# Optimization experiments

Measured on AMD Instinct MI355X. Metric: run time of the kernel, lower is better.

The kernel has to match this reference:

```python
import jax, jax.numpy as jnp
import numpy as np

N = 20000        # nodes per type (ant, user)
E = 400000       # edges per relation
F_IN = 128       # args.user_num -> input feature dim
H = 10           # attention heads
D1, D2 = 16, 32  # per-head out channels of HGT layers 1 and 2
H1, H2 = H * D1, H * D2  # 160, 320


def _segment_softmax(logit, dst, n):
    m = jax.ops.segment_max(logit, dst, num_segments=n)
    e = jnp.exp(logit - m[dst])
    s = jax.ops.segment_sum(e, dst, num_segments=n)
    return e / (s[dst] + 1e-16)


def _hgt_layer(x_a, x_u, ei_au, ea_au, ei_ua, ea_ua,
               kw, kb, qw, qb, vw, vb, arel, mrel, prel, ew, eb, alw, alb, D):
    # per-node-type K/Q/V projections, reshaped to [N, H, D]
    def proj(x, w, b, i):
        return (x @ w[i] + b[i]).reshape(x.shape[0], H, D)
    k_a, q_a, v_a = proj(x_a, kw, kb, 0), proj(x_a, qw, qb, 0), proj(x_a, vw, vb, 0)
    k_u, q_u, v_u = proj(x_u, kw, kb, 1), proj(x_u, qw, qb, 1), proj(x_u, vw, vb, 1)
    scale = 1.0 / jnp.sqrt(jnp.float32(D))

    def relation(k_s, v_s, q_d, ei, ea, r, n_dst):
        # apply per-relation matrices at node granularity (cheaper than per-edge)
        kr = jnp.einsum('nhd,hde->nhe', k_s, arel[r])
        vr = jnp.einsum('nhd,hde->nhe', v_s, mrel[r])
        src, dst = ei[0], ei[1]
        # [E, H] attention logits: HGT dot-product * relation prior + edge-attr term
        logit = (q_d[dst] * kr[src]).sum(-1) * scale * prel[r] + ea @ ew[r] + eb[r]
        a = _segment_softmax(logit, dst, n_dst)
        msg = vr[src] * a[..., None]                        # [E, H, D]
        out = jax.ops.segment_sum(msg, dst, num_segments=n_dst)
        return out.reshape(n_dst, H * D)

    agg_u = relation(k_a, v_a, q_u, ei_au, ea_au, 0, x_u.shape[0])  # ant -> user
    agg_a = relation(k_u, v_u, q_a, ei_ua, ea_ua, 1, x_a.shape[0])  # user -> ant
    out_a = jax.nn.gelu(agg_a) @ alw[0] + alb[0]
    out_u = jax.nn.gelu(agg_u) @ alw[1] + alb[1]
    return out_a, out_u


def _bn(x, g, b):
    mu = x.mean(0)
    var = x.var(0)
    return (x - mu) / jnp.sqrt(var + 1e-5) * g + b


def _forward(x_ant, x_user, ea_au, ea_ua,
             l1_kw, l1_kb, l1_qw, l1_qb, l1_vw, l1_vb, l1_arel, l1_mrel, l1_prel, l1_ew, l1_eb, l1_alw, l1_alb,
             l2_kw, l2_kb, l2_qw, l2_qb, l2_vw, l2_vb, l2_arel, l2_mrel, l2_prel, l2_ew, l2_eb, l2_alw, l2_alb,
             lin1_w, lin1_b, bn_g, bn_b, lin2_wa, lin2_ba, lin2_wu, lin2_bu,
             ei_au, ei_ua):
    a, u = _hgt_layer(x_ant, x_user, ei_au, ea_au, ei_ua, ea_ua,
                      l1_kw, l1_kb, l1_qw, l1_qb, l1_vw, l1_vb,
                      l1_arel, l1_mrel, l1_prel, l1_ew, l1_eb, l1_alw, l1_alb, D1)
    a, u = jax.nn.elu(a), jax.nn.elu(u)
    a, u = _hgt_layer(a, u, ei_au, ea_au, ei_ua, ea_ua,
                      l2_kw, l2_kb, l2_qw, l2_qb, l2_vw, l2_vb,
                      l2_arel, l2_mrel, l2_prel, l2_ew, l2_eb, l2_alw, l2_alb, D2)
    a, u = jax.nn.elu(a), jax.nn.elu(u)
    a = jax.nn.elu(a @ lin1_w[0] + lin1_b[0])
    u = jax.nn.elu(u @ lin1_w[1] + lin1_b[1])
    a = _bn(a, bn_g[0], bn_b[0])
    u = _bn(u, bn_g[1], bn_b[1])
    a = a @ lin2_wa + lin2_ba       # [N, user_num]   beamforming weights
    u = u @ lin2_wu + lin2_bu       # [N, user_num+1] assignment logits
    # MM_Dict_ACT: power-normalize ant outputs, softmax user assignments
    a = a / jnp.sqrt((a * a).sum(-1, keepdims=True) + 1e-12)
    u = jax.nn.softmax(u, axis=-1)
    return a, u


def setup_inputs() -> dict:
    key = jax.random.key(0)
    ks = iter(jax.random.split(key, 64))
    nk = lambda: next(ks)
    rn = lambda shape, s=0.05: jax.random.normal(nk(), shape, dtype=jnp.float32) * s
    inp = {}
    inp['x_ant'] = rn((N, F_IN), 1.0)
    inp['x_user'] = rn((N, F_IN), 1.0)
    inp['ea_au'] = jax.random.uniform(nk(), (E, 1), dtype=jnp.float32)
    inp['ea_ua'] = jax.random.uniform(nk(), (E, 1), dtype=jnp.float32)

    def hgt_params(p, fin, d):
        hd = H * d
        inp[p + 'kw'] = rn((2, fin, hd)); inp[p + 'kb'] = jnp.zeros((2, hd))
        inp[p + 'qw'] = rn((2, fin, hd)); inp[p + 'qb'] = jnp.zeros((2, hd))
        inp[p + 'vw'] = rn((2, fin, hd)); inp[p + 'vb'] = jnp.zeros((2, hd))
        inp[p + 'arel'] = rn((2, H, d, d), 0.2)
        inp[p + 'mrel'] = rn((2, H, d, d), 0.2)
        inp[p + 'prel'] = jnp.ones((2, H), dtype=jnp.float32)
        inp[p + 'ew'] = rn((2, 1, H)); inp[p + 'eb'] = jnp.zeros((2, H))
        inp[p + 'alw'] = rn((2, hd, hd)); inp[p + 'alb'] = jnp.zeros((2, hd))

    hgt_params('l1_', F_IN, D1)
    hgt_params('l2_', H1, D2)
    inp['lin1_w'] = rn((2, H2, 512)); inp['lin1_b'] = jnp.zeros((2, 512))
    inp['bn_g'] = jnp.ones((2, 512), dtype=jnp.float32)
    inp['bn_b'] = jnp.zeros((2, 512), dtype=jnp.float32)
    inp['lin2_wa'] = rn((512, F_IN)); inp['lin2_ba'] = jnp.zeros((F_IN,))
    inp['lin2_wu'] = rn((512, F_IN + 1)); inp['lin2_bu'] = jnp.zeros((F_IN + 1,))
    inp['ei_au'] = jax.random.randint(nk(), (2, E), 0, N)
    inp['ei_ua'] = jax.random.randint(nk(), (2, E), 0, N)
    return inp


def reference(x_ant, x_user, ea_au, ea_ua,
              l1_kw, l1_kb, l1_qw, l1_qb, l1_vw, l1_vb, l1_arel, l1_mrel, l1_prel, l1_ew, l1_eb, l1_alw, l1_alb,
              l2_kw, l2_kb, l2_qw, l2_qb, l2_vw, l2_vb, l2_arel, l2_mrel, l2_prel, l2_ew, l2_eb, l2_alw, l2_alb,
              lin1_w, lin1_b, bn_g, bn_b, lin2_wa, lin2_ba, lin2_wu, lin2_bu,
              ei_au, ei_ua):
    return _forward(x_ant, x_user, ea_au, ea_ua,
                    l1_kw, l1_kb, l1_qw, l1_qb, l1_vw, l1_vb, l1_arel, l1_mrel, l1_prel, l1_ew, l1_eb, l1_alw, l1_alb,
                    l2_kw, l2_kb, l2_qw, l2_qb, l2_vw, l2_vb, l2_arel, l2_mrel, l2_prel, l2_ew, l2_eb, l2_alw, l2_alb,
                    lin1_w, lin1_b, bn_g, bn_b, lin2_wa, lin2_ba, lin2_wu, lin2_bu,
                    ei_au, ei_ua)
```

## Files before the change

### kernel.cpp

```cpp
#include <hip/hip_runtime.h>
#include <hip/hip_bf16.h>
#include <math.h>

#define N_NODES 20000
#define N_EDGES 400000
#define NH 10

typedef __attribute__((ext_vector_type(8))) short short8v;
typedef __attribute__((ext_vector_type(4))) float f32x4;

__device__ __forceinline__ float gelu_f(float x) {
    float x3 = x * x * x;
    return 0.5f * x * (1.0f + tanhf(0.7978845608028654f * (x + 0.044715f * x3)));
}
__device__ __forceinline__ float elu_f(float x) {
    return x > 0.0f ? x : (expf(x) - 1.0f);
}
__device__ __forceinline__ float bf_lo(unsigned int w) {
    return __uint_as_float(w << 16);
}
__device__ __forceinline__ float bf_hi(unsigned int w) {
    return __uint_as_float(w & 0xffff0000u);
}
__device__ __forceinline__ unsigned short f2b(float x) {
    unsigned int u = __float_as_uint(x);
    return (unsigned short)((u + 0x7fffu + ((u >> 16) & 1u)) >> 16);
}

struct GP {
    const void *A0, *A1;
    const __hip_bfloat16 *W0, *W1;
    const float *b0, *b1;
    void *C0, *C1;
    int N0, N1;
    float* stats;
    const float *scl, *sft;
};
template<int ACT, int MODE, typename AT, typename OUT>
__global__ __launch_bounds__(256) void gemm2_kernel(GP P, int M, int K)
{
    constexpr int PITCH = 40;
    __shared__ __align__(16) unsigned short As[128 * PITCH];
    __shared__ __align__(16) unsigned short Bs[128 * PITCH];
    const int z = blockIdx.z;
    const AT* A  = (const AT*)(z ? P.A1 : P.A0);
    const __hip_bfloat16* WT = z ? P.W1 : P.W0;
    const float* bias = z ? P.b1 : P.b0;
    OUT* C = (OUT*)(z ? P.C1 : P.C0);
    const int N = z ? P.N1 : P.N0;

    const int tid = threadIdx.x;
    const int m0 = blockIdx.y * 128, n0 = blockIdx.x * 128;
    if (n0 >= N) return;
    const int w = tid >> 6, l = tid & 63;
    const int wr = w >> 1, wc = w & 1;
    const int lr = l & 15, lk = l >> 4;

    const int srow = tid >> 1, sseg = (tid & 1) * 16;
    const bool ainb = (m0 + srow) < M;
    const bool binb = (n0 + srow) < N;
    const AT* aptr = A + (size_t)(m0 + srow) * K + sseg;
    const __hip_bfloat16* bptr = WT + (size_t)(n0 + srow) * K + sseg;

    constexpr int NRA = (sizeof(AT) == 4) ? 4 : 2;
    int4 ra[NRA], rb0, rb1;
    auto ld = [&](int k0) {
        #pragma unroll
        for (int i = 0; i < NRA; ++i)
            ra[i] = ainb ? ((const int4*)(aptr + k0))[i] : make_int4(0, 0, 0, 0);
        rb0 = binb ? *(const int4*)(bptr + k0)     : make_int4(0, 0, 0, 0);
        rb1 = binb ? *(const int4*)(bptr + k0 + 8) : make_int4(0, 0, 0, 0);
    };
    auto stage = [&](int k0) {
        if constexpr (sizeof(AT) == 4) {
            const float* fv = (const float*)ra;
            unsigned int pk[8];
            #pragma unroll
            for (int q = 0; q < 8; ++q)
                pk[q] = (unsigned int)f2b(fv[2 * q]) |
                        ((unsigned int)f2b(fv[2 * q + 1]) << 16);
            *(int4*)&As[srow * PITCH + sseg]     = *(int4*)&pk[0];
            *(int4*)&As[srow * PITCH + sseg + 8] = *(int4*)&pk[4];
        } else if constexpr (MODE == 2) {
            const unsigned int* uv = (const unsigned int*)ra;
            const float* scl = P.scl + z * 512;
            const float* sft = P.sft + z * 512;
            unsigned int pk[8];
            #pragma unroll
            for (int q = 0; q < 8; ++q) {
                const int c0 = k0 + sseg + 2 * q;
                float x0 = fmaf(bf_lo(uv[q]), scl[c0], sft[c0]);
                float x1 = fmaf(bf_hi(uv[q]), scl[c0 + 1], sft[c0 + 1]);
                pk[q] = (unsigned int)f2b(x0) | ((unsigned int)f2b(x1) << 16);
            }
            *(int4*)&As[srow * PITCH + sseg]     = *(int4*)&pk[0];
            *(int4*)&As[srow * PITCH + sseg + 8] = *(int4*)&pk[4];
        } else {
            *(int4*)&As[srow * PITCH + sseg]     = ra[0];
            *(int4*)&As[srow * PITCH + sseg + 8] = ra[1];
        }
        *(int4*)&Bs[srow * PITCH + sseg]     = rb0;
        *(int4*)&Bs[srow * PITCH + sseg + 8] = rb1;
    };

    f32x4 acc[4][4] = {};
    ld(0);
    for (int k0 = 0; k0 < K; k0 += 32) {
        stage(k0);
        __syncthreads();
        if (k0 + 32 < K) ld(k0 + 32);
        short8v a[4], b[4];
        #pragma unroll
        for (int mi = 0; mi < 4; ++mi)
            a[mi] = *reinterpret_cast<const short8v*>(
                &As[(wr * 64 + mi * 16 + lr) * PITCH + lk * 8]);
        #pragma unroll
        for (int ni = 0; ni < 4; ++ni)
            b[ni] = *reinterpret_cast<const short8v*>(
                &Bs[(wc * 64 + ni * 16 + lr) * PITCH + lk * 8]);
        #pragma unroll
        for (int mi = 0; mi < 4; ++mi)
            #pragma unroll
            for (int ni = 0; ni < 4; ++ni)
                acc[mi][ni] = __builtin_amdgcn_mfma_f32_16x16x32_bf16(
                    a[mi], b[ni], acc[mi][ni], 0, 0, 0);
        __syncthreads();
    }

    float* cs = (float*)As;
    if constexpr (MODE == 1) {
        if (tid < 256) cs[tid] = 0.f;
        __syncthreads();
    }
    #pragma unroll
    for (int ni = 0; ni < 4; ++ni) {
        const int col = n0 + wc * 64 + ni * 16 + lr;
        if (col >= N) continue;
        const float bv = bias[col];
        float lsum = 0.f, lsq = 0.f;
        #pragma unroll
        for (int mi = 0; mi < 4; ++mi) {
            const int rb = m0 + wr * 64 + mi * 16 + lk * 4;
            #pragma unroll
            for (int j = 0; j < 4; ++j) {
                const int m = rb + j;
                if (m >= M) continue;
                float v = acc[mi][ni][j] + bv;
                if (ACT == 1) v = elu_f(v);
                if constexpr (MODE == 1) { lsum += v; lsq = fmaf(v, v, lsq); }
                if constexpr (sizeof(OUT) == 2)
                    C[(size_t)m * N + col] = __float2bfloat16(v);
                else
                    C[(size_t)m * N + col] = v;
            }
        }
        if constexpr (MODE == 1) {
            const int ct = wc * 64 + ni * 16 + lr;
            atomicAdd(&cs[ct], lsum);
            atomicAdd(&cs[128 + ct], lsq);
        }
    }
    if constexpr (MODE == 1) {
        __syncthreads();
        if (tid < 128) {
            const int col = n0 + tid;
            if (col < N) {
                atomicAdd(&P.stats[z * 1024 + col], cs[tid]);
                atomicAdd(&P.stats[z * 1024 + 512 + col], cs[128 + tid]);
            }
        }
    }
}

__global__ void bnprep_kernel(const float* __restrict__ S, const float* __restrict__ g,
                              const float* __restrict__ b,
                              float* __restrict__ SCL, float* __restrict__ SFT)
{
    int t = blockIdx.x * 256 + threadIdx.x;
    if (t >= 1024) return;
    const int z = t >> 9, c = t & 511;
    const float mu = S[z * 1024 + c] / (float)N_NODES;
    const float var = S[z * 1024 + 512 + c] / (float)N_NODES - mu * mu;
    const float scl = g[z * 512 + c] * rsqrtf(var + 1e-5f);
    SCL[z * 512 + c] = scl;
    SFT[z * 512 + c] = b[z * 512 + c] - mu * scl;
}

struct TJob { const float* in; __hip_bfloat16* out; int K; int N; };
struct TJobs8 { TJob j[8]; };
__global__ void transpose8_kernel(TJobs8 J)
{
    __shared__ float tile[32][33];
    const TJob job = J.j[blockIdx.z];
    const int K = job.K, N = job.N;
    const int nb = blockIdx.x * 32, kb = blockIdx.y * 32;
    if (nb >= N || kb >= K) return;
    const int tx = threadIdx.x & 31, ty = threadIdx.x >> 5;
    for (int j = ty; j < 32; j += 8) {
        int k = kb + j, n = nb + tx;
        tile[j][tx] = (k < K && n < N) ? job.in[(size_t)k * N + n] : 0.f;
    }
    __syncthreads();
    for (int j = ty; j < 32; j += 8) {
        int n = nb + j, k = kb + tx;
        if (n < N && k < K) job.out[(size_t)n * K + k] = __float2bfloat16(tile[tx][j]);
    }
}

struct PrepArgs {
    const float *qw1, *qb1, *kw1, *kb1, *vw1, *vb1, *ar1, *mr1;
    const float *qw2, *qb2, *kw2, *kb2, *vw2, *vb2, *ar2, *mr2;
    __hip_bfloat16 *W1a, *W1u, *W2a, *W2u;
    float *B1a, *B1u, *B2a, *B2u;
};
__global__ void prep_qkv4_kernel(PrepArgs A)
{
    const int y = blockIdx.y;
    const int layer = y >> 1, type = y & 1;
    const int D = layer ? 32 : 16;
    const int fin = layer ? 160 : 128;
    const int HD = NH * D;
    const float* qw = layer ? A.qw2 : A.qw1;
    const float* qb = layer ? A.qb2 : A.qb1;
    const float* kw = layer ? A.kw2 : A.kw1;
    const float* kb = layer ? A.kb2 : A.kb1;
    const float* vw = layer ? A.vw2 : A.vw1;
    const float* vb = layer ? A.vb2 : A.vb1;
    const float* ar = layer ? A.ar2 : A.ar1;
    const float* mr = layer ? A.mr2 : A.mr1;
    __hip_bfloat16* WT = layer ? (type ? A.W2u : A.W2a) : (type ? A.W1u : A.W1a);
    float* BIAS = layer ? (type ? A.B2u : A.B2a) : (type ? A.B1u : A.B1a);
    const size_t woff = (size_t)type * fin * HD;
    const size_t roff = (size_t)type * NH * D * D;

    const int F1 = fin + 1;
    int tid = blockIdx.x * blockDim.x + threadIdx.x;
    if (tid >= 3 * HD * F1) return;
    const int f = tid % F1;
    const int col3 = tid / F1;
    const int sec = col3 / HD;
    const int col = col3 - sec * HD;
    float val;
    if (sec == 0) {
        val = (f < fin) ? qw[woff + (size_t)f * HD + col] : qb[type * HD + col];
    } else {
        const float* W = (sec == 1) ? kw : vw;
        const float* B = (sec == 1) ? kb : vb;
        const float* R = ((sec == 1) ? ar : mr) + roff;
        const int h = col / D, e = col - h * D;
        const float* src = (f < fin) ? W + woff + (size_t)f * HD + h * D
                                     : B + type * HD + h * D;
        const float* r = R + (size_t)h * D * D + e;
        float acc = 0.f;
        for (int d = 0; d < D; ++d) acc = fmaf(src[d], r[(size_t)d * D], acc);
        val = acc;
    }
    if (f < fin) WT[(size_t)col3 * fin + f] = __float2bfloat16(val);
    else         BIAS[col3] = val;
}

template<int D>
__global__ __launch_bounds__(256) void edge_fused_kernel(
    const __hip_bfloat16* __restrict__ Ta, const __hip_bfloat16* __restrict__ Tu,
    const int* __restrict__ rp0, const int* __restrict__ src0, const float* __restrict__ eav0,
    const int* __restrict__ rp1, const int* __restrict__ src1, const float* __restrict__ eav1,
    const float* __restrict__ prel, const float* __restrict__ ew,
    const float* __restrict__ eb,
    __hip_bfloat16* __restrict__ outA, __hip_bfloat16* __restrict__ outU,
    float scale)
{
    constexpr int HD = NH * D;
    constexpr int S = 3 * HD;
    constexpr int C = 64;
    constexpr int POS = HD / 8;
    constexpr int G = (POS * 8 <= 256) ? 8 : 4;
    __shared__ float q_s[HD];
    __shared__ float ls[C][NH];
    __shared__ int   srcs[C];
    __shared__ float eas[C];
    __shared__ float prel_s[NH], ew_s[NH], eb_s[NH];

    const int b = blockIdx.x;
    const int rel = b & 1, dst = b >> 1;
    const int t = threadIdx.x;
    const __hip_bfloat16* Tkv = rel ? Tu : Ta;
    const __hip_bfloat16* Tq  = rel ? Ta : Tu;
    const int* rp    = rel ? rp1 : rp0;
    const int* srcA  = rel ? src1 : src0;
    const float* eav = rel ? eav1 : eav0;
    __hip_bfloat16* out = rel ? outA : outU;

    const int s0 = rp[dst], deg = rp[dst + 1] - s0;

    {
        const unsigned int* qrow = (const unsigned int*)(Tq + (size_t)dst * S);
        for (int i = t; i < HD / 2; i += 256) {
            unsigned int wd = qrow[i];
            q_s[2 * i]     = bf_lo(wd);
            q_s[2 * i + 1] = bf_hi(wd);
        }
    }
    if (t < NH) { prel_s[t] = prel[rel * NH + t]; ew_s[t] = ew[rel * NH + t];
                  eb_s[t] = eb[rel * NH + t]; }
    const int apos = t / G, ag = t % G;
    const int ah = (apos * 8) / D;
    float a8[8] = {};
    float ssum = 0.f;
    __syncthreads();

    for (int base = 0; base < deg; base += C) {
        const int cl = min(C, deg - base);
        if (t < cl) {
            srcs[t] = srcA[s0 + base + t];
            eas[t]  = eav[s0 + base + t];
        }
        __syncthreads();
        for (int item = t; item < cl * NH; item += 256) {
            const int p = item / NH, h = item - p * NH;
            const uint4* kr = (const uint4*)(Tkv + (size_t)srcs[p] * S + HD + h * D);
            const float* qh = q_s + h * D;
            float d0 = 0.f;
            #pragma unroll
            for (int c4 = 0; c4 < D / 8; ++c4) {
                const uint4 wd = kr[c4];
                const float* qq = qh + c4 * 8;
                d0 = fmaf(qq[0], bf_lo(wd.x), d0); d0 = fmaf(qq[1], bf_hi(wd.x), d0);
                d0 = fmaf(qq[2], bf_lo(wd.y), d0); d0 = fmaf(qq[3], bf_hi(wd.y), d0);
                d0 = fmaf(qq[4], bf_lo(wd.z), d0); d0 = fmaf(qq[5], bf_hi(wd.z), d0);
                d0 = fmaf(qq[6], bf_lo(wd.w), d0); d0 = fmaf(qq[7], bf_hi(wd.w), d0);
            }
            ls[p][h] = expf(d0 * scale * prel_s[h] + eas[p] * ew_s[h] + eb_s[h]);
        }
        __syncthreads();
        if (apos < POS) {
            for (int p = ag; p < cl; p += G) {
                const uint4* vr = (const uint4*)(Tkv + (size_t)srcs[p] * S + 2 * HD);
                const uint4 wd = vr[apos];
                const float wgt = ls[p][ah];
                ssum += wgt;
                a8[0] = fmaf(wgt, bf_lo(wd.x), a8[0]); a8[1] = fmaf(wgt, bf_hi(wd.x), a8[1]);
                a8[2] = fmaf(wgt, bf_lo(wd.y), a8[2]); a8[3] = fmaf(wgt, bf_hi(wd.y), a8[3]);
                a8[4] = fmaf(wgt, bf_lo(wd.z), a8[4]); a8[5] = fmaf(wgt, bf_hi(wd.z), a8[5]);
                a8[6] = fmaf(wgt, bf_lo(wd.w), a8[6]); a8[7] = fmaf(wgt, bf_hi(wd.w), a8[7]);
            }
        }
        __syncthreads();
    }
    if (apos < POS) {
        #pragma unroll
        for (int off = G / 2; off; off >>= 1) {
            #pragma unroll
            for (int j = 0; j < 8; ++j) a8[j] += __shfl_xor(a8[j], off);
            ssum += __shfl_xor(ssum, off);
        }
        if (ag == 0) {
            const float inv = 1.f / (ssum + 1e-16f);
            uint4 o;
            o.x = (unsigned int)f2b(gelu_f(a8[0] * inv)) |
                  ((unsigned int)f2b(gelu_f(a8[1] * inv)) << 16);
            o.y = (unsigned int)f2b(gelu_f(a8[2] * inv)) |
                  ((unsigned int)f2b(gelu_f(a8[3] * inv)) << 16);
            o.z = (unsigned int)f2b(gelu_f(a8[4] * inv)) |
                  ((unsigned int)f2b(gelu_f(a8[5] * inv)) << 16);
            o.w = (unsigned int)f2b(gelu_f(a8[6] * inv)) |
                  ((unsigned int)f2b(gelu_f(a8[7] * inv)) << 16);
            ((uint4*)(out + (size_t)dst * HD))[apos] = o;
        }
    }
}

__global__ void count2_kernel(const int* __restrict__ ei0, const int* __restrict__ ei1,
                              int* __restrict__ cnt0, int* __restrict__ cnt1)
{
    int e = blockIdx.x * blockDim.x + threadIdx.x;
    if (e >= N_EDGES) return;
    if (blockIdx.y == 0) atomicAdd(&cnt0[ei0[N_EDGES + e]], 1);
    else                 atomicAdd(&cnt1[ei1[N_EDGES + e]], 1);
}

__global__ void scatter2_kernel(const int* __restrict__ ei0, const float* __restrict__ ea0,
                                const int* __restrict__ ei1, const float* __restrict__ ea1,
                                int* __restrict__ cur0, int* __restrict__ cur1,
                                int* __restrict__ srcA0, float* __restrict__ eaA0,
                                int* __restrict__ srcA1, float* __restrict__ eaA1)
{
    int e = blockIdx.x * blockDim.x + threadIdx.x;
    if (e >= N_EDGES) return;
    const int y = blockIdx.y;
    const int* ei = y ? ei1 : ei0;
    const float* ea = y ? ea1 : ea0;
    int* cursor = y ? cur1 : cur0;
    int* srcA = y ? srcA1 : srcA0;
    float* eaA = y ? eaA1 : eaA0;
    int dst = ei[N_EDGES + e];
    int pos = atomicAdd(&cursor[dst], 1);
    srcA[pos] = ei[e];
    eaA[pos] = ea[e];
}

__global__ void exscan2_kernel(const int* __restrict__ cnt0, int* __restrict__ rp0, int* __restrict__ cur0,
                               const int* __restrict__ cnt1, int* __restrict__ rp1, int* __restrict__ cur1,
                               int n)
{
    __shared__ int sums[1024];
    const int* cnt = blockIdx.x ? cnt1 : cnt0;
    int* rp = blockIdx.x ? rp1 : rp0;
    int* cursor = blockIdx.x ? cur1 : cur0;
    const int t = threadIdx.x;
    const int CH = (n + 1023) / 1024;
    const int b0 = t * CH;
    int local = 0;
    for (int i = 0; i < CH; ++i) {
        int idx = b0 + i;
        if (idx < n) local += cnt[idx];
    }
    sums[t] = local;
    __syncthreads();
    for (int off = 1; off < 1024; off <<= 1) {
        int x = (t >= off) ? sums[t - off] : 0;
        __syncthreads();
        sums[t] += x;
        __syncthreads();
    }
    int run = sums[t] - local;
    for (int i = 0; i < CH; ++i) {
        int idx = b0 + i;
        if (idx < n) {
            rp[idx] = run; cursor[idx] = run;
            run += cnt[idx];
        }
    }
    if (t == 1023) rp[n] = sums[1023];
}

__global__ void epilogue_kernel(const float* __restrict__ XA, const float* __restrict__ XU,
                                float* __restrict__ out)
{
    const int row = blockIdx.x;
    const int l = threadIdx.x;
    if (blockIdx.y == 0) {
        const float* x = XA + (size_t)row * 128;
        float v0 = x[l], v1 = x[l + 64];
        float ss = v0 * v0 + v1 * v1;
        #pragma unroll
        for (int off = 32; off; off >>= 1) ss += __shfl_xor(ss, off);
        float inv = rsqrtf(ss + 1e-12f);
        out[(size_t)row * 128 + l] = v0 * inv;
        out[(size_t)row * 128 + l + 64] = v1 * inv;
    } else {
        const float* x = XU + (size_t)row * 129;
        float* o = out + (size_t)N_NODES * 128;
        float v0 = x[l], v1 = x[l + 64];
        float v2 = (l == 0) ? x[128] : -3.4e38f;
        float m = fmaxf(fmaxf(v0, v1), v2);
        #pragma unroll
        for (int off = 32; off; off >>= 1) m = fmaxf(m, __shfl_xor(m, off));
        float e0 = expf(v0 - m), e1 = expf(v1 - m);
        float e2 = (l == 0) ? expf(v2 - m) : 0.f;
        float s = e0 + e1 + e2;
        #pragma unroll
        for (int off = 32; off; off >>= 1) s += __shfl_xor(s, off);
        float inv = 1.f / s;
        o[(size_t)row * 129 + l] = e0 * inv;
        o[(size_t)row * 129 + l + 64] = e1 * inv;
        if (l == 0) o[(size_t)row * 129 + 128] = e2 * inv;
    }
}

template<int ACT, int MODE, typename AT, typename OUT>
static inline void launch_gemm2(const AT* A0, const __hip_bfloat16* W0,
                                const float* b0, OUT* C0, int N0,
                                const AT* A1, const __hip_bfloat16* W1,
                                const float* b1, OUT* C1, int N1,
                                int M, int K, hipStream_t s,
                                float* stats = nullptr,
                                const float* scl = nullptr, const float* sft = nullptr)
{
    GP P = { (const void*)A0, (const void*)A1, W0, W1, b0, b1,
             (void*)C0, (void*)C1, N0, N1, stats, scl, sft };
    const int maxN = N0 > N1 ? N0 : N1;
    dim3 grid((maxN + 127) / 128, (M + 127) / 128, 2);
    gemm2_kernel<ACT, MODE, AT, OUT><<<grid, 256, 0, s>>>(P, M, K);
}

struct LayerParams {
    const float *kw, *kb, *qw, *qb, *vw, *vb, *arel, *mrel, *prel, *ew, *eb, *alw, *alb;
};

struct CsrRel { const int* rp; const int* src; const float* eav; };

template<int D, typename AT>
static void run_layer(const LayerParams& P, int fin,
                      const AT* xa, const AT* xu,
                      __hip_bfloat16* TA, __hip_bfloat16* TU,
                      __hip_bfloat16* AGA, __hip_bfloat16* AGU,
                      __hip_bfloat16* ya, __hip_bfloat16* yu,
                      const __hip_bfloat16* WQa, const __hip_bfloat16* WQu,
                      const float* Ba, const float* Bu,
                      const __hip_bfloat16* WALa, const __hip_bfloat16* WALu,
                      const CsrRel& au, const CsrRel& ua, hipStream_t s)
{
    const int HD = NH * D;
    const float scale = 1.0f / sqrtf((float)D);

    launch_gemm2<0, 0, AT, __hip_bfloat16>(xa, WQa, Ba, TA, 3 * HD,
                                           xu, WQu, Bu, TU, 3 * HD, N_NODES, fin, s);

    edge_fused_kernel<D><<<2 * N_NODES, 256, 0, s>>>(
        TA, TU, au.rp, au.src, au.eav, ua.rp, ua.src, ua.eav,
        P.prel, P.ew, P.eb, AGA, AGU, scale);

    launch_gemm2<1, 0, __hip_bfloat16, __hip_bfloat16>(
        AGA, WALa, P.alb, ya, HD, AGU, WALu, P.alb + HD, yu, HD, N_NODES, HD, s);
}

extern "C" void kernel_launch(void* const* d_in, const int* in_sizes, int n_in,
                              void* d_out, int out_size, void* d_ws, size_t ws_size,
                              hipStream_t stream)
{
    const float* x_ant  = (const float*)d_in[0];
    const float* x_user = (const float*)d_in[1];
    const float* ea_au  = (const float*)d_in[2];
    const float* ea_ua  = (const float*)d_in[3];
    LayerParams L1 = {
        (const float*)d_in[4],  (const float*)d_in[5],  (const float*)d_in[6],
        (const float*)d_in[7],  (const float*)d_in[8],  (const float*)d_in[9],
        (const float*)d_in[10], (const float*)d_in[11], (const float*)d_in[12],
        (const float*)d_in[13], (const float*)d_in[14], (const float*)d_in[15],
        (const float*)d_in[16]
    };
    LayerParams L2 = {
        (const float*)d_in[17], (const float*)d_in[18], (const float*)d_in[19],
        (const float*)d_in[20], (const float*)d_in[21], (const float*)d_in[22],
        (const float*)d_in[23], (const float*)d_in[24], (const float*)d_in[25],
        (const float*)d_in[26], (const float*)d_in[27], (const float*)d_in[28],
        (const float*)d_in[29]
    };
    const float* lin1_w  = (const float*)d_in[30];
    const float* lin1_b  = (const float*)d_in[31];
    const float* bn_g    = (const float*)d_in[32];
    const float* bn_b    = (const float*)d_in[33];
    const float* lin2_wa = (const float*)d_in[34];
    const float* lin2_ba = (const float*)d_in[35];
    const float* lin2_wu = (const float*)d_in[36];
    const float* lin2_bu = (const float*)d_in[37];
    const int*   ei_au   = (const int*)d_in[38];
    const int*   ei_ua   = (const int*)d_in[39];

    char* P8 = (char*)d_ws;
    auto carve = [&](size_t bytes) { char* p = P8; P8 += (bytes + 255) & ~(size_t)255; return p; };
    __hip_bfloat16* TA  = (__hip_bfloat16*)carve((size_t)N_NODES * 960 * 2);
    __hip_bfloat16* TU  = (__hip_bfloat16*)carve((size_t)N_NODES * 960 * 2);
    __hip_bfloat16* AGA = (__hip_bfloat16*)carve((size_t)N_NODES * 320 * 2);
    __hip_bfloat16* AGU = (__hip_bfloat16*)carve((size_t)N_NODES * 320 * 2);
    __hip_bfloat16* YA  = (__hip_bfloat16*)carve((size_t)N_NODES * 320 * 2);
    __hip_bfloat16* YU  = (__hip_bfloat16*)carve((size_t)N_NODES * 320 * 2);
    __hip_bfloat16* L1A = (__hip_bfloat16*)carve((size_t)N_NODES * 512 * 2);
    __hip_bfloat16* L1U = (__hip_bfloat16*)carve((size_t)N_NODES * 512 * 2);
    __hip_bfloat16* WQ1A = (__hip_bfloat16*)carve(480 * 128 * 2);
    __hip_bfloat16* WQ1U = (__hip_bfloat16*)carve(480 * 128 * 2);
    __hip_bfloat16* WQ2A = (__hip_bfloat16*)carve(960 * 160 * 2);
    __hip_bfloat16* WQ2U = (__hip_bfloat16*)carve(960 * 160 * 2);
    __hip_bfloat16* WAL1A = (__hip_bfloat16*)carve(160 * 160 * 2);
    __hip_bfloat16* WAL1U = (__hip_bfloat16*)carve(160 * 160 * 2);
    __hip_bfloat16* WAL2A = (__hip_bfloat16*)carve(320 * 320 * 2);
    __hip_bfloat16* WAL2U = (__hip_bfloat16*)carve(320 * 320 * 2);
    __hip_bfloat16* WL1A = (__hip_bfloat16*)carve(512 * 320 * 2);
    __hip_bfloat16* WL1U = (__hip_bfloat16*)carve(512 * 320 * 2);
    __hip_bfloat16* WL2A = (__hip_bfloat16*)carve(128 * 512 * 2);
    __hip_bfloat16* WL2U = (__hip_bfloat16*)carve(129 * 512 * 2);
    float* B1A = (float*)carve(480 * 4);
    float* B1U = (float*)carve(480 * 4);
    float* B2A = (float*)carve(960 * 4);
    float* B2U = (float*)carve(960 * 4);
    float* STATS = (float*)carve(2048 * 4);
    float* SCL = (float*)carve(1024 * 4);
    float* SFT = (float*)carve(1024 * 4);
    int*   rp_au  = (int*)carve((N_NODES + 1) * 4);
    int*   rp_ua  = (int*)carve((N_NODES + 1) * 4);
    int*   src_au = (int*)carve((size_t)N_EDGES * 4);
    float* eav_au = (float*)carve((size_t)N_EDGES * 4);
    int*   src_ua = (int*)carve((size_t)N_EDGES * 4);
    float* eav_ua = (float*)carve((size_t)N_EDGES * 4);
    int*   cursor = (int*)carve((size_t)2 * N_NODES * 4);
    int*   counts = (int*)carve((size_t)2 * N_NODES * 4);

    const int gE = (N_EDGES + 255) / 256;

    {
        PrepArgs PA = {
            L1.qw, L1.qb, L1.kw, L1.kb, L1.vw, L1.vb, L1.arel, L1.mrel,
            L2.qw, L2.qb, L2.kw, L2.kb, L2.vw, L2.vb, L2.arel, L2.mrel,
            WQ1A, WQ1U, WQ2A, WQ2U, B1A, B1U, B2A, B2U
        };
        dim3 g((3 * 320 * 161 + 255) / 256, 4);
        prep_qkv4_kernel<<<g, 256, 0, stream>>>(PA);
    }
    {
        TJobs8 J = {{
            { L1.alw,                      WAL1A, 160, 160 },
            { L1.alw + (size_t)160 * 160,  WAL1U, 160, 160 },
            { L2.alw,                      WAL2A, 320, 320 },
            { L2.alw + (size_t)320 * 320,  WAL2U, 320, 320 },
            { lin1_w,                      WL1A,  320, 512 },
            { lin1_w + (size_t)320 * 512,  WL1U,  320, 512 },
            { lin2_wa,                     WL2A,  512, 128 },
            { lin2_wu,                     WL2U,  512, 129 }
        }};
        dim3 g(512 / 32, 512 / 32, 8);
        transpose8_kernel<<<g, 256, 0, stream>>>(J);
    }

    hipMemsetAsync(counts, 0, 2 * N_NODES * sizeof(int), stream);
    hipMemsetAsync(STATS, 0, 2048 * sizeof(float), stream);
    {
        dim3 g(gE, 2);
        count2_kernel<<<g, 256, 0, stream>>>(ei_au, ei_ua, counts, counts + N_NODES);
    }
    exscan2_kernel<<<2, 1024, 0, stream>>>(counts, rp_au, cursor,
                                           counts + N_NODES, rp_ua, cursor + N_NODES,
                                           N_NODES);
    {
        dim3 g(gE, 2);
        scatter2_kernel<<<g, 256, 0, stream>>>(ei_au, ea_au, ei_ua, ea_ua,
                                               cursor, cursor + N_NODES,
                                               src_au, eav_au, src_ua, eav_ua);
    }
    CsrRel au = { rp_au, src_au, eav_au };
    CsrRel ua = { rp_ua, src_ua, eav_ua };

    run_layer<16, float>(L1, 128, x_ant, x_user, TA, TU, AGA, AGU, YA, YU,
                         WQ1A, WQ1U, B1A, B1U, WAL1A, WAL1U, au, ua, stream);

    run_layer<32, __hip_bfloat16>(L2, 160, YA, YU, TA, TU, AGA, AGU, TA, TU,
                                  WQ2A, WQ2U, B2A, B2U, WAL2A, WAL2U, au, ua, stream);

    launch_gemm2<1, 1, __hip_bfloat16, __hip_bfloat16>(
        TA, WL1A, lin1_b, L1A, 512, TU, WL1U, lin1_b + 512, L1U, 512,
        N_NODES, 320, stream, STATS);

    bnprep_kernel<<<4, 256, 0, stream>>>(STATS, bn_g, bn_b, SCL, SFT);

    float* OUTA = (float*)AGA;
    float* OUTU = (float*)AGU;
    launch_gemm2<0, 2, __hip_bfloat16, float>(
        L1A, WL2A, lin2_ba, OUTA, 128, L1U, WL2U, lin2_bu, OUTU, 129,
        N_NODES, 512, stream, nullptr, SCL, SFT);
    {
        dim3 g(N_NODES, 2);
        epilogue_kernel<<<g, 64, 0, stream>>>(OUTA, OUTU, (float*)d_out);
    }
}
```

Before: 862.0 us.

## Merge weight prep kernels, combine memsets, process both relations per edge block

```diff
diff --git a/kernel.cpp b/kernel.cpp
--- a/kernel.cpp
+++ b/kernel.cpp
@@ -187,35 +187,35 @@
 }
 
 struct TJob { const float* in; __hip_bfloat16* out; int K; int N; };
-struct TJobs8 { TJob j[8]; };
-__global__ void transpose8_kernel(TJobs8 J)
-{
-    __shared__ float tile[32][33];
-    const TJob job = J.j[blockIdx.z];
-    const int K = job.K, N = job.N;
-    const int nb = blockIdx.x * 32, kb = blockIdx.y * 32;
-    if (nb >= N || kb >= K) return;
-    const int tx = threadIdx.x & 31, ty = threadIdx.x >> 5;
-    for (int j = ty; j < 32; j += 8) {
-        int k = kb + j, n = nb + tx;
-        tile[j][tx] = (k < K && n < N) ? job.in[(size_t)k * N + n] : 0.f;
-    }
-    __syncthreads();
-    for (int j = ty; j < 32; j += 8) {
-        int n = nb + j, k = kb + tx;
-        if (n < N && k < K) job.out[(size_t)n * K + k] = __float2bfloat16(tile[tx][j]);
-    }
-}
-
-struct PrepArgs {
+struct PrepAll {
     const float *qw1, *qb1, *kw1, *kb1, *vw1, *vb1, *ar1, *mr1;
     const float *qw2, *qb2, *kw2, *kb2, *vw2, *vb2, *ar2, *mr2;
     __hip_bfloat16 *W1a, *W1u, *W2a, *W2u;
     float *B1a, *B1u, *B2a, *B2u;
+    TJob tj[8];
 };
-__global__ void prep_qkv4_kernel(PrepArgs A)
+__global__ void prep_all_kernel(PrepAll A)
 {
     const int y = blockIdx.y;
+    if (y >= 4) {
+        __shared__ float tile[32][33];
+        const TJob job = A.tj[y - 4];
+        const int K = job.K, N = job.N;
+        const int nT = (N + 31) / 32;
+        const int kb = (blockIdx.x / nT) * 32, nb = (blockIdx.x % nT) * 32;
+        if (kb >= K) return;
+        const int tx = threadIdx.x & 31, ty = threadIdx.x >> 5;
+        for (int j = ty; j < 32; j += 8) {
+            int k = kb + j, n = nb + tx;
+            tile[j][tx] = (k < K && n < N) ? job.in[(size_t)k * N + n] : 0.f;
+        }
+        __syncthreads();
+        for (int j = ty; j < 32; j += 8) {
+            int n = nb + j, k = kb + tx;
+            if (n < N && k < K) job.out[(size_t)n * K + k] = __float2bfloat16(tile[tx][j]);
+        }
+        return;
+    }
     const int layer = y >> 1, type = y & 1;
     const int D = layer ? 32 : 16;
     const int fin = layer ? 160 : 128;
@@ -278,94 +278,96 @@
     __shared__ float ls[C][NH];
     __shared__ int   srcs[C];
     __shared__ float eas[C];
-    __shared__ float prel_s[NH], ew_s[NH], eb_s[NH];
-
-    const int b = blockIdx.x;
-    const int rel = b & 1, dst = b >> 1;
+    __shared__ float prel_s[2 * NH], ew_s[2 * NH], eb_s[2 * NH];
+
+    const int dst = blockIdx.x;
     const int t = threadIdx.x;
-    const __hip_bfloat16* Tkv = rel ? Tu : Ta;
-    const __hip_bfloat16* Tq  = rel ? Ta : Tu;
-    const int* rp    = rel ? rp1 : rp0;
-    const int* srcA  = rel ? src1 : src0;
-    const float* eav = rel ? eav1 : eav0;
-    __hip_bfloat16* out = rel ? outA : outU;
-
-    const int s0 = rp[dst], deg = rp[dst + 1] - s0;
-
-    {
-        const unsigned int* qrow = (const unsigned int*)(Tq + (size_t)dst * S);
-        for (int i = t; i < HD / 2; i += 256) {
-            unsigned int wd = qrow[i];
-            q_s[2 * i]     = bf_lo(wd);
-            q_s[2 * i + 1] = bf_hi(wd);
-        }
-    }
-    if (t < NH) { prel_s[t] = prel[rel * NH + t]; ew_s[t] = ew[rel * NH + t];
-                  eb_s[t] = eb[rel * NH + t]; }
+    if (t < 2 * NH) { prel_s[t] = prel[t]; ew_s[t] = ew[t]; eb_s[t] = eb[t]; }
     const int apos = t / G, ag = t % G;
     const int ah = (apos * 8) / D;
-    float a8[8] = {};
-    float ssum = 0.f;
-    __syncthreads();
-
-    for (int base = 0; base < deg; base += C) {
-        const int cl = min(C, deg - base);
-        if (t < cl) {
-            srcs[t] = srcA[s0 + base + t];
-            eas[t]  = eav[s0 + base + t];
-        }
-        __syncthreads();
-        for (int item = t; item < cl * NH; item += 256) {
-            const int p = item / NH, h = item - p * NH;
-            const uint4* kr = (const uint4*)(Tkv + (size_t)srcs[p] * S + HD + h * D);
-            const float* qh = q_s + h * D;
-            float d0 = 0.f;
+
+    for (int rel = 0; rel < 2; ++rel) {
+        const __hip_bfloat16* Tkv = rel ? Tu : Ta;
+        const __hip_bfloat16* Tq  = rel ? Ta : Tu;
+        const int* rp    = rel ? rp1 : rp0;
+        const int* srcA  = rel ? src1 : src0;
+        const float* eav = rel ? eav1 : eav0;
+        __hip_bfloat16* out = rel ? outA : outU;
+        const int s0 = rp[dst], deg = rp[dst + 1] - s0;
+
+        {
+            const unsigned int* qrow = (const unsigned int*)(Tq + (size_t)dst * S);
+            for (int i = t; i < HD / 2; i += 256) {
+                unsigned int wd = qrow[i];
+                q_s[2 * i]     = bf_lo(wd);
+                q_s[2 * i + 1] = bf_hi(wd);
+            }
+        }
+        float a8[8] = {};
+        float ssum = 0.f;
+        __syncthreads();
+
+        for (int base = 0; base < deg; base += C) {
+            const int cl = min(C, deg - base);
+            if (t < cl) {
+                srcs[t] = srcA[s0 + base + t];
+                eas[t]  = eav[s0 + base + t];
+            }
+            __syncthreads();
+            for (int item = t; item < cl * NH; item += 256) {
+                const int p = item / NH, h = item - p * NH;
+                const uint4* kr = (const uint4*)(Tkv + (size_t)srcs[p] * S + HD + h * D);
+                const float* qh = q_s + h * D;
+                float d0 = 0.f;
+                #pragma unroll
+                for (int c4 = 0; c4 < D / 8; ++c4) {
+                    const uint4 wd = kr[c4];
+                    const float* qq = qh + c4 * 8;
+                    d0 = fmaf(qq[0], bf_lo(wd.x), d0); d0 = fmaf(qq[1], bf_hi(wd.x), d0);
+                    d0 = fmaf(qq[2], bf_lo(wd.y), d0); d0 = fmaf(qq[3], bf_hi(wd.y), d0);
+                    d0 = fmaf(qq[4], bf_lo(wd.z), d0); d0 = fmaf(qq[5], bf_hi(wd.z), d0);
+                    d0 = fmaf(qq[6], bf_lo(wd.w), d0); d0 = fmaf(qq[7], bf_hi(wd.w), d0);
+                }
+                ls[p][h] = expf(d0 * scale * prel_s[rel * NH + h]
+                                + eas[p] * ew_s[rel * NH + h] + eb_s[rel * NH + h]);
+            }
+            __syncthreads();
+            if (apos < POS) {
+                for (int p = ag; p < cl; p += G) {
+                    const uint4* vr = (const uint4*)(Tkv + (size_t)srcs[p] * S + 2 * HD);
+                    const uint4 wd = vr[apos];
+                    const float wgt = ls[p][ah];
+                    ssum += wgt;
+                    a8[0] = fmaf(wgt, bf_lo(wd.x), a8[0]); a8[1] = fmaf(wgt, bf_hi(wd.x), a8[1]);
+                    a8[2] = fmaf(wgt, bf_lo(wd.y), a8[2]); a8[3] = fmaf(wgt, bf_hi(wd.y), a8[3]);
+                    a8[4] = fmaf(wgt, bf_lo(wd.z), a8[4]); a8[5] = fmaf(wgt, bf_hi(wd.z), a8[5]);
+                    a8[6] = fmaf(wgt, bf_lo(wd.w), a8[6]); a8[7] = fmaf(wgt, bf_hi(wd.w), a8[7]);
+                }
+            }
+            __syncthreads();
+        }
+        if (apos < POS) {
             #pragma unroll
-            for (int c4 = 0; c4 < D / 8; ++c4) {
-                const uint4 wd = kr[c4];
-                const float* qq = qh + c4 * 8;
-                d0 = fmaf(qq[0], bf_lo(wd.x), d0); d0 = fmaf(qq[1], bf_hi(wd.x), d0);
-                d0 = fmaf(qq[2], bf_lo(wd.y), d0); d0 = fmaf(qq[3], bf_hi(wd.y), d0);
-                d0 = fmaf(qq[4], bf_lo(wd.z), d0); d0 = fmaf(qq[5], bf_hi(wd.z), d0);
-                d0 = fmaf(qq[6], bf_lo(wd.w), d0); d0 = fmaf(qq[7], bf_hi(wd.w), d0);
-            }
-            ls[p][h] = expf(d0 * scale * prel_s[h] + eas[p] * ew_s[h] + eb_s[h]);
-        }
-        __syncthreads();
-        if (apos < POS) {
-            for (int p = ag; p < cl; p += G) {
-                const uint4* vr = (const uint4*)(Tkv + (size_t)srcs[p] * S + 2 * HD);
-                const uint4 wd = vr[apos];
-                const float wgt = ls[p][ah];
-                ssum += wgt;
-                a8[0] = fmaf(wgt, bf_lo(wd.x), a8[0]); a8[1] = fmaf(wgt, bf_hi(wd.x), a8[1]);
-                a8[2] = fmaf(wgt, bf_lo(wd.y), a8[2]); a8[3] = fmaf(wgt, bf_hi(wd.y), a8[3]);
-                a8[4] = fmaf(wgt, bf_lo(wd.z), a8[4]); a8[5] = fmaf(wgt, bf_hi(wd.z), a8[5]);
-                a8[6] = fmaf(wgt, bf_lo(wd.w), a8[6]); a8[7] = fmaf(wgt, bf_hi(wd.w), a8[7]);
-            }
-        }
-        __syncthreads();
-    }
-    if (apos < POS) {
-        #pragma unroll
-        for (int off = G / 2; off; off >>= 1) {
-            #pragma unroll
-            for (int j = 0; j < 8; ++j) a8[j] += __shfl_xor(a8[j], off);
-            ssum += __shfl_xor(ssum, off);
-        }
-        if (ag == 0) {
-            const float inv = 1.f / (ssum + 1e-16f);
-            uint4 o;
-            o.x = (unsigned int)f2b(gelu_f(a8[0] * inv)) |
-                  ((unsigned int)f2b(gelu_f(a8[1] * inv)) << 16);
-            o.y = (unsigned int)f2b(gelu_f(a8[2] * inv)) |
-                  ((unsigned int)f2b(gelu_f(a8[3] * inv)) << 16);
-            o.z = (unsigned int)f2b(gelu_f(a8[4] * inv)) |
-                  ((unsigned int)f2b(gelu_f(a8[5] * inv)) << 16);
-            o.w = (unsigned int)f2b(gelu_f(a8[6] * inv)) |
-                  ((unsigned int)f2b(gelu_f(a8[7] * inv)) << 16);
-            ((uint4*)(out + (size_t)dst * HD))[apos] = o;
-        }
+            for (int off = G / 2; off; off >>= 1) {
+                #pragma unroll
+                for (int j = 0; j < 8; ++j) a8[j] += __shfl_xor(a8[j], off);
+                ssum += __shfl_xor(ssum, off);
+            }
+            if (ag == 0) {
+                const float inv = 1.f / (ssum + 1e-16f);
+                uint4 o;
+                o.x = (unsigned int)f2b(gelu_f(a8[0] * inv)) |
+                      ((unsigned int)f2b(gelu_f(a8[1] * inv)) << 16);
+                o.y = (unsigned int)f2b(gelu_f(a8[2] * inv)) |
+                      ((unsigned int)f2b(gelu_f(a8[3] * inv)) << 16);
+                o.z = (unsigned int)f2b(gelu_f(a8[4] * inv)) |
+                      ((unsigned int)f2b(gelu_f(a8[5] * inv)) << 16);
+                o.w = (unsigned int)f2b(gelu_f(a8[6] * inv)) |
+                      ((unsigned int)f2b(gelu_f(a8[7] * inv)) << 16);
+                ((uint4*)(out + (size_t)dst * HD))[apos] = o;
+            }
+        }
+        __syncthreads();
     }
 }
 
@@ -506,7 +508,7 @@
     launch_gemm2<0, 0, AT, __hip_bfloat16>(xa, WQa, Ba, TA, 3 * HD,
                                            xu, WQu, Bu, TU, 3 * HD, N_NODES, fin, s);
 
-    edge_fused_kernel<D><<<2 * N_NODES, 256, 0, s>>>(
+    edge_fused_kernel<D><<<N_NODES, 256, 0, s>>>(
         TA, TU, au.rp, au.src, au.eav, ua.rp, ua.src, ua.eav,
         P.prel, P.ew, P.eb, AGA, AGU, scale);
 
@@ -573,7 +575,6 @@
     float* B1U = (float*)carve(480 * 4);
     float* B2A = (float*)carve(960 * 4);
     float* B2U = (float*)carve(960 * 4);
-    float* STATS = (float*)carve(2048 * 4);
     float* SCL = (float*)carve(1024 * 4);
     float* SFT = (float*)carve(1024 * 4);
     int*   rp_au  = (int*)carve((N_NODES + 1) * 4);
@@ -584,35 +585,29 @@
     float* eav_ua = (float*)carve((size_t)N_EDGES * 4);
     int*   cursor = (int*)carve((size_t)2 * N_NODES * 4);
     int*   counts = (int*)carve((size_t)2 * N_NODES * 4);
+    float* STATS  = (float*)carve(2048 * 4);
 
     const int gE = (N_EDGES + 255) / 256;
 
     {
-        PrepArgs PA = {
+        PrepAll PA = {
             L1.qw, L1.qb, L1.kw, L1.kb, L1.vw, L1.vb, L1.arel, L1.mrel,
             L2.qw, L2.qb, L2.kw, L2.kb, L2.vw, L2.vb, L2.arel, L2.mrel,
-            WQ1A, WQ1U, WQ2A, WQ2U, B1A, B1U, B2A, B2U
+            WQ1A, WQ1U, WQ2A, WQ2U, B1A, B1U, B2A, B2U,
+            {{ L1.alw,                      WAL1A, 160, 160 },
+             { L1.alw + (size_t)160 * 160,  WAL1U, 160, 160 },
+             { L2.alw,                      WAL2A, 320, 320 },
+             { L2.alw + (size_t)320 * 320,  WAL2U, 320, 320 },
+             { lin1_w,                      WL1A,  320, 512 },
+             { lin1_w + (size_t)320 * 512,  WL1U,  320, 512 },
+             { lin2_wa,                     WL2A,  512, 128 },
+             { lin2_wu,                     WL2U,  512, 129 }}
         };
-        dim3 g((3 * 320 * 161 + 255) / 256, 4);
-        prep_qkv4_kernel<<<g, 256, 0, stream>>>(PA);
-    }
-    {
-        TJobs8 J = {{
-            { L1.alw,                      WAL1A, 160, 160 },
-            { L1.alw + (size_t)160 * 160,  WAL1U, 160, 160 },
-            { L2.alw,                      WAL2A, 320, 320 },
-            { L2.alw + (size_t)320 * 320,  WAL2U, 320, 320 },
-            { lin1_w,                      WL1A,  320, 512 },
-            { lin1_w + (size_t)320 * 512,  WL1U,  320, 512 },
-            { lin2_wa,                     WL2A,  512, 128 },
-            { lin2_wu,                     WL2U,  512, 129 }
-        }};
-        dim3 g(512 / 32, 512 / 32, 8);
-        transpose8_kernel<<<g, 256, 0, stream>>>(J);
-    }
-
-    hipMemsetAsync(counts, 0, 2 * N_NODES * sizeof(int), stream);
-    hipMemsetAsync(STATS, 0, 2048 * sizeof(float), stream);
+        dim3 g((3 * 320 * 161 + 255) / 256, 12);
+        prep_all_kernel<<<g, 256, 0, stream>>>(PA);
+    }
+
+    hipMemsetAsync(counts, 0, 2 * N_NODES * sizeof(int) + 2048 * sizeof(float), stream);
     {
         dim3 g(gE, 2);
         count2_kernel<<<g, 256, 0, stream>>>(ei_au, ei_ua, counts, counts + N_NODES);
```

After: 840.6 us. -2.5%, faster.
